# Kernel tuning notes

Hardware: AMD Instinct MI355X
Metric: run time of the kernel (lower is better)

## Reference

```python
import jax, jax.numpy as jnp
import numpy as np
import math

B, NQ, NK = 8, 1024, 2048
DQ = DK = DV = 1024
H = 8
DH = DV // H
EPS = 1e-5


def _layernorm(x, g, b):
    mu = jnp.mean(x, axis=-1, keepdims=True)
    var = jnp.mean(jnp.square(x - mu), axis=-1, keepdims=True)
    return (x - mu) * jax.lax.rsqrt(var + EPS) * g + b


def setup_inputs() -> dict:
    key = jax.random.key(0)
    ks = jax.random.split(key, 12)
    s_q = 1.0 / math.sqrt(DQ)
    s_v = 1.0 / math.sqrt(DV)
    return {
        "Q": jax.random.normal(ks[0], (B, NQ, DQ), jnp.float32),
        "K": jax.random.normal(ks[1], (B, NK, DK), jnp.float32),
        "Wq": jax.random.normal(ks[2], (DQ, DV), jnp.float32) * s_q,
        "bq": jnp.zeros((DV,), jnp.float32),
        "Wk": jax.random.normal(ks[3], (DK, DV), jnp.float32) * s_q,
        "bk": jnp.zeros((DV,), jnp.float32),
        "Wv": jax.random.normal(ks[4], (DK, DV), jnp.float32) * s_q,
        "bv": jnp.zeros((DV,), jnp.float32),
        "Wo": jax.random.normal(ks[5], (DV, DV), jnp.float32) * s_v,
        "bo": jnp.zeros((DV,), jnp.float32),
        "g0": jnp.ones((DV,), jnp.float32),
        "b0": jnp.zeros((DV,), jnp.float32),
        "g1": jnp.ones((DV,), jnp.float32),
        "b1": jnp.zeros((DV,), jnp.float32),
    }


def reference(Q, K, Wq, bq, Wk, bk, Wv, bv, Wo, bo, g0, b0, g1, b1):
    # projections
    q = Q @ Wq + bq                      # [B, NQ, DV]
    k = K @ Wk + bk                      # [B, NK, DV]
    v = K @ Wv + bv                      # [B, NK, DV]
    qh = q.reshape(B, NQ, H, DH)
    kh = k.reshape(B, NK, H, DH)
    vh = v.reshape(B, NK, H, DH)
    # NOTE: original scales by sqrt(dim_V), not sqrt(d_head)
    scale = 1.0 / math.sqrt(DV)
    logits = jnp.einsum("bqhd,bkhd->bhqk", qh, kh) * scale
    A = jax.nn.softmax(logits, axis=-1)
    # residual baked into attention output: Q_ + A @ V_
    Oh = qh + jnp.einsum("bhqk,bkhd->bqhd", A, vh)
    O = Oh.reshape(B, NQ, DV)
    O = _layernorm(O, g0, b0)
    O = O + jax.nn.relu(O @ Wo + bo)
    O = _layernorm(O, g1, b1)
    return O
```

## Files before the change

kernel.cpp:

```cpp
#include <hip/hip_runtime.h>
#include <stdint.h>

#define DEVI static __device__ __forceinline__

typedef __attribute__((ext_vector_type(8))) short short8;
typedef __attribute__((ext_vector_type(4))) float floatx4;
typedef __attribute__((ext_vector_type(4))) unsigned short ushortx4;

DEVI unsigned short f2bf(float f) {
  union { float f; uint32_t u; } v; v.f = f;
  uint32_t r = v.u + 0x7FFFu + ((v.u >> 16) & 1u);
  return (unsigned short)(r >> 16);
}
DEVI float bf2f(unsigned short s) {
  union { uint32_t u; float f; } v; v.u = ((uint32_t)s) << 16;
  return v.f;
}

DEVI void lds_cp16(void* lds, const void* g) {
  __builtin_amdgcn_global_load_lds(
      (const __attribute__((address_space(1))) uint32_t*)g,
      reinterpret_cast<__attribute__((address_space(3))) uint32_t*>(
          (uint32_t)reinterpret_cast<uintptr_t>(lds)),
      16, 0, 0);
}

__global__ __launch_bounds__(256) void cvt_bf16(const float* __restrict__ X,
                                                unsigned short* __restrict__ Y) {
  const size_t i = (size_t)blockIdx.x * 256 + threadIdx.x;
  const floatx4 v = ((const floatx4*)X)[i];
  ushortx4 o;
  o.x = f2bf(v.x); o.y = f2bf(v.y); o.z = f2bf(v.z); o.w = f2bf(v.w);
  ((ushortx4*)Y)[i] = o;
}

__global__ __launch_bounds__(256) void wtrans4(const float* __restrict__ Wq,
                                               const float* __restrict__ Wk,
                                               const float* __restrict__ Wv,
                                               const float* __restrict__ Wo,
                                               unsigned short* __restrict__ Wt) {
  __shared__ float t[32][33];
  const int tx = threadIdx.x, ty = threadIdx.y;
  const int z = blockIdx.z;
  const float* W = (z == 0) ? Wq : (z == 1) ? Wk : (z == 2) ? Wv : Wo;
  unsigned short* D = Wt + (size_t)z * 1024 * 1024;
  const int c0 = blockIdx.x * 32, r0 = blockIdx.y * 32;
#pragma unroll
  for (int i = 0; i < 4; i++)
    t[ty + i * 8][tx] = W[(size_t)(r0 + ty + i * 8) * 1024 + c0 + tx];
  __syncthreads();
#pragma unroll
  for (int i = 0; i < 4; i++)
    D[(size_t)(c0 + ty + i * 8) * 1024 + r0 + tx] = f2bf(t[tx][ty + i * 8]);
}

template <int EPI>
__global__ __launch_bounds__(256, 3) void gemm_bt(
    const unsigned short* __restrict__ A, const unsigned short* __restrict__ Bt,
    const float* __restrict__ bias, void* __restrict__ Cout) {
  __shared__ unsigned short As[2][4][128][8];
  __shared__ unsigned short Bs[2][4][128][8];

  const int tid = threadIdx.x;
  const int lane = tid & 63, w = tid >> 6;
  const int wr = w >> 1, wc = w & 1;
  const int qd = lane >> 4, l16 = lane & 15;
  const int m0 = blockIdx.y * 128, n0 = blockIdx.x * 128;

  floatx4 acc[4][4];
#pragma unroll
  for (int i = 0; i < 4; i++)
#pragma unroll
    for (int j = 0; j < 4; j++) { floatx4 z = {0.f, 0.f, 0.f, 0.f}; acc[i][j] = z; }

  const int prow = tid & 127;
  const unsigned short* aptr = A + (size_t)(m0 + prow) * 1024 + ((tid >> 7) << 3);
  const unsigned short* bptr = Bt + (size_t)(n0 + prow) * 1024 + ((tid >> 7) << 3);
  const int dstoff = tid * 8;

  lds_cp16(&As[0][0][0][0] + dstoff, aptr);
  lds_cp16(&As[0][0][0][0] + dstoff + 2048, aptr + 16);
  lds_cp16(&Bs[0][0][0][0] + dstoff, bptr);
  lds_cp16(&Bs[0][0][0][0] + dstoff + 2048, bptr + 16);

  for (int it = 0; it < 32; it++) {
    __syncthreads();
    if (it < 31) {
      const int nb = (it + 1) & 1, k0 = (it + 1) * 32;
      lds_cp16(&As[nb][0][0][0] + dstoff, aptr + k0);
      lds_cp16(&As[nb][0][0][0] + dstoff + 2048, aptr + k0 + 16);
      lds_cp16(&Bs[nb][0][0][0] + dstoff, bptr + k0);
      lds_cp16(&Bs[nb][0][0][0] + dstoff + 2048, bptr + k0 + 16);
    }
    const int cur = it & 1;
    short8 af[4], bf[4];
#pragma unroll
    for (int mi = 0; mi < 4; mi++)
      af[mi] = *(const short8*)&As[cur][qd][wr * 64 + mi * 16 + l16][0];
#pragma unroll
    for (int ni = 0; ni < 4; ni++)
      bf[ni] = *(const short8*)&Bs[cur][qd][wc * 64 + ni * 16 + l16][0];
#pragma unroll
    for (int mi = 0; mi < 4; mi++)
#pragma unroll
      for (int ni = 0; ni < 4; ni++)
        acc[mi][ni] =
            __builtin_amdgcn_mfma_f32_16x16x32_bf16(af[mi], bf[ni], acc[mi][ni], 0, 0, 0);
  }

#pragma unroll
  for (int mi = 0; mi < 4; mi++) {
#pragma unroll
    for (int ni = 0; ni < 4; ni++) {
      const int row = m0 + wr * 64 + mi * 16 + qd * 4;
      const int col = n0 + wc * 64 + ni * 16 + l16;
      const float bv = bias[col];
      if constexpr (EPI == 0) {
        unsigned short* C = (unsigned short*)Cout;
#pragma unroll
        for (int r = 0; r < 4; r++)
          C[(size_t)(row + r) * 1024 + col] = f2bf(acc[mi][ni][r] + bv);
      } else {
        float* C = (float*)Cout;
#pragma unroll
        for (int r = 0; r < 4; r++)
          C[(size_t)(row + r) * 1024 + col] = acc[mi][ni][r] + bv;
      }
    }
  }
}

__global__ __launch_bounds__(256, 3) void gemm_kv(
    const unsigned short* __restrict__ A, const unsigned short* __restrict__ Bt,
    const float* __restrict__ biasK, const float* __restrict__ biasV,
    unsigned short* __restrict__ CK, unsigned short* __restrict__ CV) {
  __shared__ unsigned short As[2][4][256][8];
  __shared__ unsigned short Bs[2][4][128][8];

  const int tid = threadIdx.x;
  const int lane = tid & 63, w = tid >> 6;
  const int wr = w >> 1, wc = w & 1;
  const int qd = lane >> 4, l16 = lane & 15;
  const int m0 = blockIdx.y * 256, n0 = blockIdx.x * 128;

  floatx4 acc[8][4];
#pragma unroll
  for (int i = 0; i < 8; i++)
#pragma unroll
    for (int j = 0; j < 4; j++) { floatx4 z = {0.f, 0.f, 0.f, 0.f}; acc[i][j] = z; }

  const unsigned short* aptr = A + (size_t)(m0 + tid) * 1024;
  const int brow = tid & 127, bc0 = tid >> 7;
  const unsigned short* bptr = Bt + (size_t)(n0 + brow) * 1024 + bc0 * 8;

#pragma unroll
  for (int c = 0; c < 4; c++) lds_cp16(&As[0][c][tid][0], aptr + c * 8);
  lds_cp16(&Bs[0][bc0][brow][0], bptr);
  lds_cp16(&Bs[0][bc0 + 2][brow][0], bptr + 16);

  for (int it = 0; it < 32; it++) {
    __syncthreads();
    if (it < 31) {
      const int nb = (it + 1) & 1, k0 = (it + 1) * 32;
#pragma unroll
      for (int c = 0; c < 4; c++) lds_cp16(&As[nb][c][tid][0], aptr + k0 + c * 8);
      lds_cp16(&Bs[nb][bc0][brow][0], bptr + k0);
      lds_cp16(&Bs[nb][bc0 + 2][brow][0], bptr + k0 + 16);
    }
    const int cur = it & 1;
    short8 af[8], bf[4];
#pragma unroll
    for (int mi = 0; mi < 8; mi++)
      af[mi] = *(const short8*)&As[cur][qd][wr * 128 + mi * 16 + l16][0];
#pragma unroll
    for (int ni = 0; ni < 4; ni++)
      bf[ni] = *(const short8*)&Bs[cur][qd][wc * 64 + ni * 16 + l16][0];
#pragma unroll
    for (int mi = 0; mi < 8; mi++)
#pragma unroll
      for (int ni = 0; ni < 4; ni++)
        acc[mi][ni] =
            __builtin_amdgcn_mfma_f32_16x16x32_bf16(af[mi], bf[ni], acc[mi][ni], 0, 0, 0);
  }

#pragma unroll
  for (int mi = 0; mi < 8; mi++) {
#pragma unroll
    for (int ni = 0; ni < 4; ni++) {
      const int row = m0 + wr * 128 + mi * 16 + qd * 4;
      const int col = n0 + wc * 64 + ni * 16 + l16;
      if (col < 1024) {
        const float bv = biasK[col];
#pragma unroll
        for (int r = 0; r < 4; r++)
          CK[(size_t)(row + r) * 1024 + col] = f2bf(acc[mi][ni][r] + bv);
      } else {
        const int vc = col - 1024;
        const float bv = biasV[vc];
        const int bb = row >> 11, nk = row & 2047;
        const int hh = vc >> 7, dh = vc & 127;
        ushortx4 pk;
        pk.x = f2bf(acc[mi][ni][0] + bv);
        pk.y = f2bf(acc[mi][ni][1] + bv);
        pk.z = f2bf(acc[mi][ni][2] + bv);
        pk.w = f2bf(acc[mi][ni][3] + bv);
        *(ushortx4*)&CV[(size_t)((bb * 8 + hh) * 128 + dh) * 2048 + nk] = pk;
      }
    }
  }
}

__global__ __launch_bounds__(256, 2) void attn(
    const unsigned short* __restrict__ qb, const unsigned short* __restrict__ kb,
    const unsigned short* __restrict__ vt, unsigned short* __restrict__ Ob) {
  __shared__ unsigned short smem[32768];

  const int tid = threadIdx.x;
  const int lane = tid & 63, w = tid >> 6;
  const int qd = lane >> 4, l16 = lane & 15;
  const int bid = blockIdx.x;
  const int qt = bid >> 6, bh = bid & 63;
  const int h = bh >> 3, b = bh & 7;
  const int m0 = qt * 128;

  const size_t qbase = ((size_t)(b * 1024 + m0)) * 1024 + h * 128;
  const size_t kbase = ((size_t)(b * 2048)) * 1024 + h * 128;
  const size_t vbase = ((size_t)((b * 8 + h) * 128)) * 2048;

#pragma unroll
  for (int i = 0; i < 8; i++) {
    const int p = i * 256 + tid;
    const int row = p & 127, c = p >> 7;
    lds_cp16(&smem[c * 1024 + row * 8], qb + qbase + (size_t)row * 1024 + c * 8);
  }
#pragma unroll
  for (int i = 0; i < 2; i++) {
    const int p = i * 256 + tid;
    const int kr = p & 31, kc = p >> 5;
    lds_cp16(&smem[16384 + kc * 256 + kr * 8], kb + kbase + (size_t)kr * 1024 + kc * 8);
    const int dh = p & 127, vc = p >> 7;
    lds_cp16(&smem[24576 + vc * 1024 + dh * 8], vt + vbase + (size_t)dh * 2048 + vc * 8);
  }
  __syncthreads();

  short8 qf[2][4];
#pragma unroll
  for (int mi = 0; mi < 2; mi++)
#pragma unroll
    for (int ks = 0; ks < 4; ks++)
      qf[mi][ks] =
          *(const short8*)&smem[(ks * 4 + qd) * 1024 + ((w * 2 + mi) * 16 + l16) * 8];
  __syncthreads();

  floatx4 oacc[2][8];
#pragma unroll
  for (int mi = 0; mi < 2; mi++)
#pragma unroll
    for (int ni = 0; ni < 8; ni++) { floatx4 z = {0.f, 0.f, 0.f, 0.f}; oacc[mi][ni] = z; }
  float lsum[2][4];
#pragma unroll
  for (int mi = 0; mi < 2; mi++)
#pragma unroll
    for (int r = 0; r < 4; r++) lsum[mi][r] = 0.f;

  for (int it = 0; it < 64; it++) {
    if (it) __syncthreads();
    if (it + 1 < 64) {
      const int nb = (it + 1) & 1, kv0 = (it + 1) * 32;
#pragma unroll
      for (int i = 0; i < 2; i++) {
        const int p = i * 256 + tid;
        const int kr = p & 31, kc = p >> 5;
        lds_cp16(&smem[16384 + nb * 4096 + kc * 256 + kr * 8],
                 kb + kbase + (size_t)(kv0 + kr) * 1024 + kc * 8);
        const int dh = p & 127, vc = p >> 7;
        lds_cp16(&smem[24576 + nb * 4096 + vc * 1024 + dh * 8],
                 vt + vbase + (size_t)dh * 2048 + kv0 + vc * 8);
      }
    }
    const int cur = it & 1;

    floatx4 sacc[2][2];
#pragma unroll
    for (int mi = 0; mi < 2; mi++)
#pragma unroll
      for (int ni = 0; ni < 2; ni++) { floatx4 z = {0.f, 0.f, 0.f, 0.f}; sacc[mi][ni] = z; }
#pragma unroll
    for (int ks = 0; ks < 4; ks++) {
      short8 b0 = *(const short8*)&smem[16384 + cur * 4096 + (ks * 4 + qd) * 256 + l16 * 8];
      short8 b1 =
          *(const short8*)&smem[16384 + cur * 4096 + (ks * 4 + qd) * 256 + (16 + l16) * 8];
#pragma unroll
      for (int mi = 0; mi < 2; mi++) {
        sacc[mi][0] = __builtin_amdgcn_mfma_f32_16x16x32_bf16(qf[mi][ks], b0, sacc[mi][0], 0, 0, 0);
        sacc[mi][1] = __builtin_amdgcn_mfma_f32_16x16x32_bf16(qf[mi][ks], b1, sacc[mi][1], 0, 0, 0);
      }
    }

#pragma unroll
    for (int mi = 0; mi < 2; mi++)
#pragma unroll
      for (int ni = 0; ni < 2; ni++) {
        const int kvl = ni * 16 + l16;
#pragma unroll
        for (int r = 0; r < 4; r++) {
          const float e = __expf(sacc[mi][ni][r] * 0.03125f);
          lsum[mi][r] += e;
          smem[(kvl >> 3) * 1024 + ((w * 2 + mi) * 16 + qd * 4 + r) * 8 + (kvl & 7)] = f2bf(e);
        }
      }

    short8 pf[2];
#pragma unroll
    for (int mi = 0; mi < 2; mi++)
      pf[mi] = *(const short8*)&smem[qd * 1024 + ((w * 2 + mi) * 16 + l16) * 8];
#pragma unroll
    for (int ni = 0; ni < 8; ni++) {
      const short8 vf = *(const short8*)&smem[24576 + cur * 4096 + qd * 1024 + (ni * 16 + l16) * 8];
#pragma unroll
      for (int mi = 0; mi < 2; mi++)
        oacc[mi][ni] = __builtin_amdgcn_mfma_f32_16x16x32_bf16(pf[mi], vf, oacc[mi][ni], 0, 0, 0);
    }
  }

  float inv[2][4];
#pragma unroll
  for (int mi = 0; mi < 2; mi++)
#pragma unroll
    for (int r = 0; r < 4; r++) {
      float s = lsum[mi][r];
      s += __shfl_xor(s, 1); s += __shfl_xor(s, 2);
      s += __shfl_xor(s, 4); s += __shfl_xor(s, 8);
      inv[mi][r] = 1.f / s;
    }

#pragma unroll
  for (int mi = 0; mi < 2; mi++)
#pragma unroll
    for (int ni = 0; ni < 8; ni++)
#pragma unroll
      for (int r = 0; r < 4; r++) {
        const int m = (w * 2 + mi) * 16 + qd * 4 + r;
        const int dh = ni * 16 + l16;
        const float qv = bf2f(qb[qbase + (size_t)m * 1024 + dh]);
        Ob[qbase + (size_t)m * 1024 + dh] = f2bf(qv + oacc[mi][ni][r] * inv[mi][r]);
      }
}

__global__ __launch_bounds__(256) void ln_rows(const unsigned short* __restrict__ X,
                                               const float* __restrict__ g,
                                               const float* __restrict__ bb,
                                               unsigned short* __restrict__ Y) {
  __shared__ float red[8];
  const int row = blockIdx.x, tid = threadIdx.x;
  const int w = tid >> 6, lane = tid & 63;
  const ushortx4 u = ((const ushortx4*)(X + (size_t)row * 1024))[tid];
  float x0 = bf2f(u.x), x1 = bf2f(u.y), x2 = bf2f(u.z), x3 = bf2f(u.w);
  float s = x0 + x1 + x2 + x3;
  float s2 = x0 * x0 + x1 * x1 + x2 * x2 + x3 * x3;
#pragma unroll
  for (int off = 1; off < 64; off <<= 1) { s += __shfl_xor(s, off); s2 += __shfl_xor(s2, off); }
  if (lane == 0) { red[w] = s; red[4 + w] = s2; }
  __syncthreads();
  s = red[0] + red[1] + red[2] + red[3];
  s2 = red[4] + red[5] + red[6] + red[7];
  const float mu = s * (1.f / 1024.f);
  const float rs = rsqrtf(s2 * (1.f / 1024.f) - mu * mu + 1e-5f);
  const floatx4 gv = ((const floatx4*)g)[tid];
  const floatx4 bv = ((const floatx4*)bb)[tid];
  ushortx4 o;
  o.x = f2bf((x0 - mu) * rs * gv.x + bv.x);
  o.y = f2bf((x1 - mu) * rs * gv.y + bv.y);
  o.z = f2bf((x2 - mu) * rs * gv.z + bv.z);
  o.w = f2bf((x3 - mu) * rs * gv.w + bv.w);
  ((ushortx4*)(Y + (size_t)row * 1024))[tid] = o;
}

__global__ __launch_bounds__(256) void final_fuse(const unsigned short* __restrict__ X1,
                                                  const float* __restrict__ Yf,
                                                  const float* __restrict__ g,
                                                  const float* __restrict__ bb,
                                                  float* __restrict__ out) {
  __shared__ float red[8];
  const int row = blockIdx.x, tid = threadIdx.x;
  const int w = tid >> 6, lane = tid & 63;
  const ushortx4 u = ((const ushortx4*)(X1 + (size_t)row * 1024))[tid];
  const floatx4 yv = ((const floatx4*)(Yf + (size_t)row * 1024))[tid];
  float x0 = bf2f(u.x) + fmaxf(yv.x, 0.f);
  float x1 = bf2f(u.y) + fmaxf(yv.y, 0.f);
  float x2 = bf2f(u.z) + fmaxf(yv.z, 0.f);
  float x3 = bf2f(u.w) + fmaxf(yv.w, 0.f);
  float s = x0 + x1 + x2 + x3;
  float s2 = x0 * x0 + x1 * x1 + x2 * x2 + x3 * x3;
#pragma unroll
  for (int off = 1; off < 64; off <<= 1) { s += __shfl_xor(s, off); s2 += __shfl_xor(s2, off); }
  if (lane == 0) { red[w] = s; red[4 + w] = s2; }
  __syncthreads();
  s = red[0] + red[1] + red[2] + red[3];
  s2 = red[4] + red[5] + red[6] + red[7];
  const float mu = s * (1.f / 1024.f);
  const float rs = rsqrtf(s2 * (1.f / 1024.f) - mu * mu + 1e-5f);
  const floatx4 gv = ((const floatx4*)g)[tid];
  const floatx4 bv = ((const floatx4*)bb)[tid];
  floatx4 o;
  o.x = (x0 - mu) * rs * gv.x + bv.x;
  o.y = (x1 - mu) * rs * gv.y + bv.y;
  o.z = (x2 - mu) * rs * gv.z + bv.z;
  o.w = (x3 - mu) * rs * gv.w + bv.w;
  ((floatx4*)(out + (size_t)row * 1024))[tid] = o;
}

extern "C" void kernel_launch(void* const* d_in, const int* in_sizes, int n_in,
                              void* d_out, int out_size, void* d_ws, size_t ws_size,
                              hipStream_t stream) {
  (void)in_sizes; (void)n_in; (void)out_size; (void)ws_size;
  const float* Q  = (const float*)d_in[0];
  const float* K  = (const float*)d_in[1];
  const float* Wq = (const float*)d_in[2];
  const float* bq = (const float*)d_in[3];
  const float* Wk = (const float*)d_in[4];
  const float* bk = (const float*)d_in[5];
  const float* Wv = (const float*)d_in[6];
  const float* bv = (const float*)d_in[7];
  const float* Wo = (const float*)d_in[8];
  const float* bo = (const float*)d_in[9];
  const float* g0 = (const float*)d_in[10];
  const float* b0 = (const float*)d_in[11];
  const float* g1 = (const float*)d_in[12];
  const float* b1 = (const float*)d_in[13];
  float* out = (float*)d_out;

  char* ws = (char*)d_ws;
  const size_t MB = 1u << 20;
  unsigned short* Qb  = (unsigned short*)(ws + 0);
  unsigned short* Kb  = (unsigned short*)(ws + 16 * MB);
  unsigned short* Wt  = (unsigned short*)(ws + 48 * MB);
  unsigned short* qbp = (unsigned short*)(ws + 56 * MB);
  unsigned short* kbp = (unsigned short*)(ws + 72 * MB);
  unsigned short* vtp = (unsigned short*)(ws + 104 * MB);
  unsigned short* O   = Qb;
  unsigned short* X1  = Kb;
  float* Yf = (float*)(ws + 72 * MB);

  unsigned short* Wqt  = Wt;
  unsigned short* Wkvt = Wt + (size_t)1024 * 1024;
  unsigned short* Wot  = Wt + (size_t)3072 * 1024;

  cvt_bf16<<<8192, 256, 0, stream>>>(Q, Qb);
  cvt_bf16<<<16384, 256, 0, stream>>>(K, Kb);
  wtrans4<<<dim3(32, 32, 4), dim3(32, 8), 0, stream>>>(Wq, Wk, Wv, Wo, Wt);

  gemm_bt<0><<<dim3(8, 64), 256, 0, stream>>>(Qb, Wqt, bq, qbp);
  gemm_kv<<<dim3(16, 64), 256, 0, stream>>>(Kb, Wkvt, bk, bv, kbp, vtp);
  attn<<<512, 256, 0, stream>>>(qbp, kbp, vtp, O);
  ln_rows<<<8192, 256, 0, stream>>>(O, g0, b0, X1);
  gemm_bt<1><<<dim3(8, 64), 256, 0, stream>>>(X1, Wot, bo, Yf);
  final_fuse<<<8192, 256, 0, stream>>>(X1, Yf, g1, b1, out);
}
```

Measured before the change: 493.9 us.

## Fuse residual-ReLU into output GEMM, enlarge KV GEMM tile, remap blocks per XCD

Several changes land together. The two fp32-to-bf16 conversion launches become one kernel. The output projection GEMM now applies ReLU and adds the residual in its epilogue, so the final kernel only does the LayerNorm. The K/V projection GEMM moves to 512 threads with a 256x256 tile to get more reuse per LDS load. Both GEMMs use a 1D grid remapped so that neighbouring M tiles land on the same XCD for L2 locality. The trade-off is a larger per-block LDS footprint in gemm_kv and an extra bf16 read of X1 inside the GEMM epilogue.

```diff
diff --git a/kernel.cpp b/kernel.cpp
--- a/kernel.cpp
+++ b/kernel.cpp
@@ -25,13 +25,20 @@
       16, 0, 0);
 }
 
-__global__ __launch_bounds__(256) void cvt_bf16(const float* __restrict__ X,
-                                                unsigned short* __restrict__ Y) {
-  const size_t i = (size_t)blockIdx.x * 256 + threadIdx.x;
-  const floatx4 v = ((const floatx4*)X)[i];
+__global__ __launch_bounds__(256) void cvt_qk(const float* __restrict__ Q,
+                                              const float* __restrict__ K,
+                                              unsigned short* __restrict__ Qb,
+                                              unsigned short* __restrict__ Kb) {
+  const int bid = blockIdx.x;
+  const float* src;
+  unsigned short* dst;
+  size_t i;
+  if (bid < 8192) { src = Q; dst = Qb; i = (size_t)bid * 256 + threadIdx.x; }
+  else            { src = K; dst = Kb; i = (size_t)(bid - 8192) * 256 + threadIdx.x; }
+  const floatx4 v = ((const floatx4*)src)[i];
   ushortx4 o;
   o.x = f2bf(v.x); o.y = f2bf(v.y); o.z = f2bf(v.z); o.w = f2bf(v.w);
-  ((ushortx4*)Y)[i] = o;
+  ((ushortx4*)dst)[i] = o;
 }
 
 __global__ __launch_bounds__(256) void wtrans4(const float* __restrict__ Wq,
@@ -57,7 +64,8 @@
 template <int EPI>
 __global__ __launch_bounds__(256, 3) void gemm_bt(
     const unsigned short* __restrict__ A, const unsigned short* __restrict__ Bt,
-    const float* __restrict__ bias, void* __restrict__ Cout) {
+    const float* __restrict__ bias, const unsigned short* __restrict__ X1,
+    void* __restrict__ Cout) {
   __shared__ unsigned short As[2][4][128][8];
   __shared__ unsigned short Bs[2][4][128][8];
 
@@ -65,7 +73,10 @@
   const int lane = tid & 63, w = tid >> 6;
   const int wr = w >> 1, wc = w & 1;
   const int qd = lane >> 4, l16 = lane & 15;
-  const int m0 = blockIdx.y * 128, n0 = blockIdx.x * 128;
+  const int bid = blockIdx.x;
+  const int xcd = bid & 7, loc = bid >> 3;
+  const int m0 = (xcd * 8 + (loc & 7)) * 128;
+  const int n0 = (loc >> 3) * 128;
 
   floatx4 acc[4][4];
 #pragma unroll
@@ -123,25 +134,30 @@
       } else {
         float* C = (float*)Cout;
 #pragma unroll
-        for (int r = 0; r < 4; r++)
-          C[(size_t)(row + r) * 1024 + col] = acc[mi][ni][r] + bv;
-      }
-    }
-  }
-}
-
-__global__ __launch_bounds__(256, 3) void gemm_kv(
+        for (int r = 0; r < 4; r++) {
+          const float x1 = bf2f(X1[(size_t)(row + r) * 1024 + col]);
+          C[(size_t)(row + r) * 1024 + col] = x1 + fmaxf(acc[mi][ni][r] + bv, 0.f);
+        }
+      }
+    }
+  }
+}
+
+__global__ __launch_bounds__(512, 2) void gemm_kv(
     const unsigned short* __restrict__ A, const unsigned short* __restrict__ Bt,
     const float* __restrict__ biasK, const float* __restrict__ biasV,
     unsigned short* __restrict__ CK, unsigned short* __restrict__ CV) {
   __shared__ unsigned short As[2][4][256][8];
-  __shared__ unsigned short Bs[2][4][128][8];
+  __shared__ unsigned short Bs[2][4][256][8];
 
   const int tid = threadIdx.x;
   const int lane = tid & 63, w = tid >> 6;
-  const int wr = w >> 1, wc = w & 1;
+  const int wr = w & 1, wc = w >> 1;
   const int qd = lane >> 4, l16 = lane & 15;
-  const int m0 = blockIdx.y * 256, n0 = blockIdx.x * 128;
+  const int bid = blockIdx.x;
+  const int xcd = bid & 7, loc = bid >> 3;
+  const int m0 = (xcd * 8 + (loc & 7)) * 256;
+  const int n0 = (loc >> 3) * 256;
 
   floatx4 acc[8][4];
 #pragma unroll
@@ -149,23 +165,25 @@
 #pragma unroll
     for (int j = 0; j < 4; j++) { floatx4 z = {0.f, 0.f, 0.f, 0.f}; acc[i][j] = z; }
 
-  const unsigned short* aptr = A + (size_t)(m0 + tid) * 1024;
-  const int brow = tid & 127, bc0 = tid >> 7;
-  const unsigned short* bptr = Bt + (size_t)(n0 + brow) * 1024 + bc0 * 8;
-
-#pragma unroll
-  for (int c = 0; c < 4; c++) lds_cp16(&As[0][c][tid][0], aptr + c * 8);
-  lds_cp16(&Bs[0][bc0][brow][0], bptr);
-  lds_cp16(&Bs[0][bc0 + 2][brow][0], bptr + 16);
+  const int r0 = tid & 255, c0 = tid >> 8;
+  const unsigned short* aptr = A + (size_t)(m0 + r0) * 1024 + c0 * 8;
+  const unsigned short* bptr = Bt + (size_t)(n0 + r0) * 1024 + c0 * 8;
+  unsigned short* dstA = &As[0][c0][r0][0];
+  unsigned short* dstB = &Bs[0][c0][r0][0];
+
+  lds_cp16(dstA, aptr);
+  lds_cp16(dstA + 4096, aptr + 16);
+  lds_cp16(dstB, bptr);
+  lds_cp16(dstB + 4096, bptr + 16);
 
   for (int it = 0; it < 32; it++) {
     __syncthreads();
     if (it < 31) {
       const int nb = (it + 1) & 1, k0 = (it + 1) * 32;
-#pragma unroll
-      for (int c = 0; c < 4; c++) lds_cp16(&As[nb][c][tid][0], aptr + k0 + c * 8);
-      lds_cp16(&Bs[nb][bc0][brow][0], bptr + k0);
-      lds_cp16(&Bs[nb][bc0 + 2][brow][0], bptr + k0 + 16);
+      lds_cp16(dstA + nb * 8192, aptr + k0);
+      lds_cp16(dstA + nb * 8192 + 4096, aptr + k0 + 16);
+      lds_cp16(dstB + nb * 8192, bptr + k0);
+      lds_cp16(dstB + nb * 8192 + 4096, bptr + k0 + 16);
     }
     const int cur = it & 1;
     short8 af[8], bf[4];
@@ -376,20 +394,15 @@
   ((ushortx4*)(Y + (size_t)row * 1024))[tid] = o;
 }
 
-__global__ __launch_bounds__(256) void final_fuse(const unsigned short* __restrict__ X1,
-                                                  const float* __restrict__ Yf,
-                                                  const float* __restrict__ g,
-                                                  const float* __restrict__ bb,
-                                                  float* __restrict__ out) {
+__global__ __launch_bounds__(256) void ln_f32(const float* __restrict__ X,
+                                              const float* __restrict__ g,
+                                              const float* __restrict__ bb,
+                                              float* __restrict__ out) {
   __shared__ float red[8];
   const int row = blockIdx.x, tid = threadIdx.x;
   const int w = tid >> 6, lane = tid & 63;
-  const ushortx4 u = ((const ushortx4*)(X1 + (size_t)row * 1024))[tid];
-  const floatx4 yv = ((const floatx4*)(Yf + (size_t)row * 1024))[tid];
-  float x0 = bf2f(u.x) + fmaxf(yv.x, 0.f);
-  float x1 = bf2f(u.y) + fmaxf(yv.y, 0.f);
-  float x2 = bf2f(u.z) + fmaxf(yv.z, 0.f);
-  float x3 = bf2f(u.w) + fmaxf(yv.w, 0.f);
+  const floatx4 xv = ((const floatx4*)(X + (size_t)row * 1024))[tid];
+  float x0 = xv.x, x1 = xv.y, x2 = xv.z, x3 = xv.w;
   float s = x0 + x1 + x2 + x3;
   float s2 = x0 * x0 + x1 * x1 + x2 * x2 + x3 * x3;
 #pragma unroll
@@ -440,20 +453,19 @@
   unsigned short* vtp = (unsigned short*)(ws + 104 * MB);
   unsigned short* O   = Qb;
   unsigned short* X1  = Kb;
-  float* Yf = (float*)(ws + 72 * MB);
+  float* O2 = (float*)(ws + 72 * MB);
 
   unsigned short* Wqt  = Wt;
   unsigned short* Wkvt = Wt + (size_t)1024 * 1024;
   unsigned short* Wot  = Wt + (size_t)3072 * 1024;
 
-  cvt_bf16<<<8192, 256, 0, stream>>>(Q, Qb);
-  cvt_bf16<<<16384, 256, 0, stream>>>(K, Kb);
+  cvt_qk<<<24576, 256, 0, stream>>>(Q, K, Qb, Kb);
   wtrans4<<<dim3(32, 32, 4), dim3(32, 8), 0, stream>>>(Wq, Wk, Wv, Wo, Wt);
 
-  gemm_bt<0><<<dim3(8, 64), 256, 0, stream>>>(Qb, Wqt, bq, qbp);
-  gemm_kv<<<dim3(16, 64), 256, 0, stream>>>(Kb, Wkvt, bk, bv, kbp, vtp);
+  gemm_bt<0><<<512, 256, 0, stream>>>(Qb, Wqt, bq, nullptr, qbp);
+  gemm_kv<<<512, 512, 0, stream>>>(Kb, Wkvt, bk, bv, kbp, vtp);
   attn<<<512, 256, 0, stream>>>(qbp, kbp, vtp, O);
   ln_rows<<<8192, 256, 0, stream>>>(O, g0, b0, X1);
-  gemm_bt<1><<<dim3(8, 64), 256, 0, stream>>>(X1, Wot, bo, Yf);
-  final_fuse<<<8192, 256, 0, stream>>>(X1, Yf, g1, b1, out);
-}
+  gemm_bt<2><<<512, 256, 0, stream>>>(X1, Wot, bo, X1, O2);
+  ln_f32<<<8192, 256, 0, stream>>>(O2, g1, b1, out);
+}
```

New measurement: 478.7 us. 3.1% less time.
